# Kernel tuning notes

Measured on AMD Instinct MI355X. Metric: run time of the kernel, lower is better.

## Reference

```python
import jax, jax.numpy as jnp
import numpy as np

D_MODEL = 256
NS = 8


def _linear_params(key, out_f, in_f):
    s = 1.0 / np.sqrt(in_f)
    kw, kb = jax.random.split(key)
    W = jax.random.uniform(kw, (out_f, in_f), jnp.float32, -s, s)
    b = jax.random.uniform(kb, (out_f,), jnp.float32, -s, s)
    return W, b


def setup_inputs() -> dict:
    key = jax.random.key(0)
    ks = jax.random.split(key, 8)
    B, NQ = 2, 10000
    C, D, H, W = D_MODEL, 16, 64, 64
    Wdp, bdp = _linear_params(ks[3], NS * 3, D_MODEL)
    Wa, ba = _linear_params(ks[4], NS, D_MODEL)
    Wv, bv = _linear_params(ks[5], D_MODEL, D_MODEL)
    Ww, bw = _linear_params(ks[6], D_MODEL, D_MODEL)
    Wo, bo = _linear_params(ks[7], D_MODEL, D_MODEL)
    return {
        "query": jax.random.normal(ks[0], (B, NQ, D_MODEL), jnp.float32),
        "ref_points": jax.random.uniform(ks[1], (B, NQ, 3), jnp.float32, -1.0, 1.0),
        "image_features": jax.random.normal(ks[2], (B, C, D, H, W), jnp.float32),
        "mask": jnp.ones((B, 2, NQ), dtype=bool),
        "Wdp": Wdp, "bdp": bdp,
        "Wa": Wa, "ba": ba,
        "Wv": Wv, "bv": bv,
        "Ww": Ww, "bw": bw,
        "Wo": Wo, "bo": bo,
    }


def grid_sample_3d(vol, grid):
    """Trilinear grid_sample, align_corners=True, zero padding.
    vol: (B,C,D,H,W); grid: (B,N,P,3) with (x,y,z) in [-1,1] (x indexes W).
    Returns (B,N,P,C)."""
    B, C, D, H, W = vol.shape
    vol_t = jnp.transpose(vol, (0, 2, 3, 4, 1))  # (B,D,H,W,C)
    ix = (grid[..., 0] + 1.0) * 0.5 * (W - 1)
    iy = (grid[..., 1] + 1.0) * 0.5 * (H - 1)
    iz = (grid[..., 2] + 1.0) * 0.5 * (D - 1)
    x0 = jnp.floor(ix); y0 = jnp.floor(iy); z0 = jnp.floor(iz)
    fx = ix - x0; fy = iy - y0; fz = iz - z0

    def gather(v, zi, yi, xi):  # v: (D,H,W,C); indices (N,P)
        return v[zi, yi, xi]  # (N,P,C)

    out = jnp.zeros(grid.shape[:-1] + (C,), vol.dtype)
    for dz in (0, 1):
        for dy in (0, 1):
            for dx in (0, 1):
                xi = x0 + dx; yi = y0 + dy; zi = z0 + dz
                w = ((fx if dx else 1.0 - fx)
                     * (fy if dy else 1.0 - fy)
                     * (fz if dz else 1.0 - fz))
                valid = ((xi >= 0) & (xi <= W - 1)
                         & (yi >= 0) & (yi <= H - 1)
                         & (zi >= 0) & (zi <= D - 1))
                xc = jnp.clip(xi, 0, W - 1).astype(jnp.int32)
                yc = jnp.clip(yi, 0, H - 1).astype(jnp.int32)
                zc = jnp.clip(zi, 0, D - 1).astype(jnp.int32)
                vals = jax.vmap(gather)(vol_t, zc, yc, xc)  # (B,N,P,C)
                out = out + (w * valid)[..., None] * vals
    return out


def reference(query, ref_points, image_features, mask,
              Wdp, bdp, Wa, ba, Wv, bv, Ww, bw, Wo, bo):
    B, NQ, C = query.shape
    n_points = NS
    # learned offsets around reference points
    delta_p = (query @ Wdp.T + bdp).reshape(B, NQ, n_points, 3)
    p_delta_p = ref_points[:, :, None, :] + delta_p
    # reorder dims [1,0,2] -> grid (x,y,z) convention of grid_sample
    grid = p_delta_p[..., jnp.array([1, 0, 2])]
    sampled = grid_sample_3d(image_features, grid)  # (B,NQ,Ns,C)
    v = sampled @ Wv.T + bv          # value_proj
    wv = v @ Ww.T + bw               # W
    attn = jax.nn.softmax(query @ Wa.T + ba, axis=-1)  # (B,NQ,Ns)
    summed = jnp.einsum('bnpc,bnp->bnc', wv, attn)
    m = jnp.any(mask, axis=1)  # (B,NQ)
    summed = summed * m[..., None]
    return summed @ Wo.T + bo
```

## Files before the change

### kernel.cpp

```cpp
#include <hip/hip_runtime.h>

#define NQ    10000
#define BATCH 2
#define CDIM  256
#define DD    16
#define HH    64
#define WW    64

using bf16x8 = __attribute__((ext_vector_type(8))) short;
using f32x4  = __attribute__((ext_vector_type(4))) float;

__device__ __forceinline__ unsigned short f2bf(float f) {
    unsigned int u = __float_as_uint(f);
    u = u + 0x7FFFu + ((u >> 16) & 1u);
    return (unsigned short)(u >> 16);
}
__device__ __forceinline__ float bf2f(unsigned short h) {
    return __uint_as_float(((unsigned int)h) << 16);
}

__global__ __launch_bounds__(256) void k_transpose_bf16(const float* __restrict__ vol,
                                                        unsigned short* __restrict__ volt) {
    __shared__ float tile[64][65];
    int bid  = blockIdx.x;
    int cblk = bid & 3;
    int y    = (bid >> 2) & 63;
    int z    = (bid >> 8) & 15;
    int b    = bid >> 12;
    int tid  = threadIdx.x;
    int lx   = tid & 63, wy = tid >> 6;

    const float* src = vol + (size_t)(b * CDIM + cblk * 64) * (DD * HH * WW)
                           + (size_t)z * (HH * WW) + y * WW;
#pragma unroll
    for (int i = 0; i < 16; ++i) {
        int cl = wy * 16 + i;
        tile[cl][lx] = src[(size_t)cl * (DD * HH * WW) + lx];
    }
    __syncthreads();
    unsigned int* dst32 = reinterpret_cast<unsigned int*>(
        volt + ((size_t)(b * DD + z) * HH + y) * WW * CDIM) + cblk * 32;
    int cp = tid & 31;
#pragma unroll
    for (int i = 0; i < 8; ++i) {
        int x = i * 8 + (tid >> 5);
        unsigned int uo = (unsigned int)f2bf(tile[cp * 2][x])
                        | ((unsigned int)f2bf(tile[cp * 2 + 1][x]) << 16);
        dst32[(size_t)x * (CDIM / 2) + cp] = uo;
    }
}

template <bool BF16OUT>
__global__ __launch_bounds__(256) void k_combine(const float* __restrict__ A,
                                                 const float* __restrict__ B,
                                                 const float* __restrict__ bin,
                                                 const float* __restrict__ badd,
                                                 void* __restrict__ outW,
                                                 float* __restrict__ outb) {
    int i = blockIdx.x, j = threadIdx.x;
    __shared__ __align__(16) float row[256];
    __shared__ float red[4];
    row[j] = A[i * 256 + j];
    __syncthreads();
    float a0 = 0.f, a1 = 0.f, a2 = 0.f, a3 = 0.f;
#pragma unroll 4
    for (int k = 0; k < 256; k += 4) {
        a0 = fmaf(row[k + 0], B[(k + 0) * 256 + j], a0);
        a1 = fmaf(row[k + 1], B[(k + 1) * 256 + j], a1);
        a2 = fmaf(row[k + 2], B[(k + 2) * 256 + j], a2);
        a3 = fmaf(row[k + 3], B[(k + 3) * 256 + j], a3);
    }
    float acc = (a0 + a1) + (a2 + a3);
    if (BF16OUT)
        ((unsigned short*)outW)[i * 256 + j] = f2bf(acc);
    else
        ((float*)outW)[i * 256 + j] = acc;

    float pb = row[j] * bin[j];
    for (int off = 32; off; off >>= 1) pb += __shfl_down(pb, off, 64);
    int lane = j & 63, wv_ = j >> 6;
    if (lane == 0) red[wv_] = pb;
    __syncthreads();
    if (j == 0) outb[i] = red[0] + red[1] + red[2] + red[3] + badd[i];
}

__device__ __forceinline__ void geom_issue(
    int p, const float* __restrict__ dotsw, const float* __restrict__ bdp,
    float r0, float r1, float r2, float a,
    const ushort4* __restrict__ vb4, int lane,
    ushort4 (&u)[8], float (&wt)[8]) {
    float ix = fmaf(r1 + dotsw[p * 3 + 1] + bdp[p * 3 + 1], 31.5f, 31.5f);
    float iy = fmaf(r0 + dotsw[p * 3 + 0] + bdp[p * 3 + 0], 31.5f, 31.5f);
    float iz = fmaf(r2 + dotsw[p * 3 + 2] + bdp[p * 3 + 2], 7.5f, 7.5f);
    float xf = floorf(ix), yf = floorf(iy), zf = floorf(iz);
    float fx = ix - xf, fy = iy - yf, fz = iz - zf;
    int x0 = (int)xf, y0 = (int)yf, z0 = (int)zf;
    int xc[2], yc[2], zc[2];
    float wx[2], wy2[2], wz2[2];
#pragma unroll
    for (int d = 0; d < 2; ++d) {
        int xi = x0 + d, yi = y0 + d, zi = z0 + d;
        wx[d]  = (xi >= 0 && xi < WW) ? (d ? fx : 1.f - fx) : 0.f;
        wy2[d] = (yi >= 0 && yi < HH) ? (d ? fy : 1.f - fy) : 0.f;
        wz2[d] = ((zi >= 0 && zi < DD) ? (d ? fz : 1.f - fz) : 0.f) * a;
        xc[d] = min(max(xi, 0), WW - 1);
        yc[d] = min(max(yi, 0), HH - 1);
        zc[d] = min(max(zi, 0), DD - 1);
    }
    float wzy[4];
#pragma unroll
    for (int zz = 0; zz < 2; ++zz)
#pragma unroll
        for (int yy = 0; yy < 2; ++yy) wzy[zz * 2 + yy] = wz2[zz] * wy2[yy];
#pragma unroll
    for (int c = 0; c < 8; ++c) {
        int dz = c >> 2, dy = (c >> 1) & 1, dx = c & 1;
        wt[c] = wzy[dz * 2 + dy] * wx[dx];
        int off = (zc[dz] * HH + yc[dy]) * WW + xc[dx];
        off = __builtin_amdgcn_readfirstlane(off);
        u[c] = vb4[(size_t)off * (CDIM / 4) + lane];
    }
}

__device__ __forceinline__ void proc8(const ushort4 (&u)[8], const float (&wt)[8],
                                      float4& acc) {
#pragma unroll
    for (int c = 0; c < 8; ++c) {
        acc.x = fmaf(wt[c], bf2f(u[c].x), acc.x);
        acc.y = fmaf(wt[c], bf2f(u[c].y), acc.y);
        acc.z = fmaf(wt[c], bf2f(u[c].z), acc.z);
        acc.w = fmaf(wt[c], bf2f(u[c].w), acc.w);
    }
}

template <bool USE_VOLT>
__global__ __launch_bounds__(256) void k_sample4(
    const float* __restrict__ query, const float* __restrict__ refp,
    const float* __restrict__ vol, const unsigned short* __restrict__ voltb,
    const float* __restrict__ Wdp, const float* __restrict__ bdp,
    const float* __restrict__ Wa, const float* __restrict__ ba,
    unsigned short* __restrict__ S) {
    int tid = threadIdx.x, w = tid >> 6, lane = tid & 63;
    int g = lane >> 4, ch = lane & 15;
    int bq0 = blockIdx.x * 4;
    __shared__ float dots[4][32];

    {
        float4 qv[4][4];
#pragma unroll
        for (int q = 0; q < 4; ++q)
#pragma unroll
            for (int i = 0; i < 4; ++i)
                qv[q][i] = *reinterpret_cast<const float4*>(
                    query + (size_t)(bq0 + q) * 256 + ch * 16 + i * 4);
#pragma unroll
        for (int rr = 0; rr < 2; ++rr) {
            int row = w * 8 + rr * 4 + g;
            const float* rp = (row < 24) ? (Wdp + row * 256) : (Wa + (row - 24) * 256);
            float4 wv4[4];
#pragma unroll
            for (int i = 0; i < 4; ++i)
                wv4[i] = *reinterpret_cast<const float4*>(rp + ch * 16 + i * 4);
#pragma unroll
            for (int q = 0; q < 4; ++q) {
                float s = 0.f;
#pragma unroll
                for (int i = 0; i < 4; ++i)
                    s = fmaf(wv4[i].x, qv[q][i].x, fmaf(wv4[i].y, qv[q][i].y,
                        fmaf(wv4[i].z, qv[q][i].z, fmaf(wv4[i].w, qv[q][i].w, s))));
                s += __shfl_xor(s, 1); s += __shfl_xor(s, 2);
                s += __shfl_xor(s, 4); s += __shfl_xor(s, 8);
                if (ch == q) dots[q][row] = s;
            }
        }
    }
    __syncthreads();

    int bq = bq0 + w, b = bq / NQ;
    const float* dotsw = dots[w];
    float lg[8]; float mx = -1e30f;
#pragma unroll
    for (int p = 0; p < 8; ++p) { lg[p] = dotsw[24 + p] + ba[p]; mx = fmaxf(mx, lg[p]); }
    float se = 0.f;
#pragma unroll
    for (int p = 0; p < 8; ++p) { lg[p] = __expf(lg[p] - mx); se += lg[p]; }
    float inv = 1.f / se;
    float r0 = refp[bq * 3 + 0], r1 = refp[bq * 3 + 1], r2 = refp[bq * 3 + 2];

    float4 acc = make_float4(0.f, 0.f, 0.f, 0.f);
    if (USE_VOLT) {
        const ushort4* vb4 = reinterpret_cast<const ushort4*>(
            voltb + (size_t)b * (DD * HH * WW) * CDIM);
        ushort4 u0[8], u1[8];
        float w0a[8], w1a[8];
        geom_issue(0, dotsw, bdp, r0, r1, r2, lg[0] * inv, vb4, lane, u0, w0a);
#pragma unroll
        for (int p = 0; p < 7; ++p) {
            if ((p & 1) == 0) {
                geom_issue(p + 1, dotsw, bdp, r0, r1, r2, lg[p + 1] * inv, vb4, lane, u1, w1a);
                proc8(u0, w0a, acc);
            } else {
                geom_issue(p + 1, dotsw, bdp, r0, r1, r2, lg[p + 1] * inv, vb4, lane, u0, w0a);
                proc8(u1, w1a, acc);
            }
        }
        proc8(u1, w1a, acc);
    } else {
        const float* vf = vol + (size_t)b * CDIM * (DD * HH * WW);
#pragma unroll
        for (int p = 0; p < 8; ++p) {
            float a = lg[p] * inv;
            float ix = fmaf(r1 + dotsw[p * 3 + 1] + bdp[p * 3 + 1], 31.5f, 31.5f);
            float iy = fmaf(r0 + dotsw[p * 3 + 0] + bdp[p * 3 + 0], 31.5f, 31.5f);
            float iz = fmaf(r2 + dotsw[p * 3 + 2] + bdp[p * 3 + 2], 7.5f, 7.5f);
            float xf = floorf(ix), yf = floorf(iy), zf = floorf(iz);
            float fx = ix - xf, fy = iy - yf, fz = iz - zf;
            int x0 = (int)xf, y0 = (int)yf, z0 = (int)zf;
            int xc[2], yc[2], zc[2]; float wx[2], wy2[2], wz2[2];
#pragma unroll
            for (int d = 0; d < 2; ++d) {
                int xi = x0 + d, yi = y0 + d, zi = z0 + d;
                wx[d]  = (xi >= 0 && xi < WW) ? (d ? fx : 1.f - fx) : 0.f;
                wy2[d] = (yi >= 0 && yi < HH) ? (d ? fy : 1.f - fy) : 0.f;
                wz2[d] = ((zi >= 0 && zi < DD) ? (d ? fz : 1.f - fz) : 0.f) * a;
                xc[d] = min(max(xi, 0), WW - 1);
                yc[d] = min(max(yi, 0), HH - 1);
                zc[d] = min(max(zi, 0), DD - 1);
            }
#pragma unroll
            for (int c = 0; c < 8; ++c) {
                int dz = c >> 2, dy = (c >> 1) & 1, dx = c & 1;
                float wgt = wz2[dz] * wy2[dy] * wx[dx];
                int off = (zc[dz] * HH + yc[dy]) * WW + xc[dx];
#pragma unroll
                for (int cc = 0; cc < 4; ++cc) {
                    float v = vf[(size_t)(lane * 4 + cc) * (DD * HH * WW) + off];
                    (&acc.x)[cc] = fmaf(wgt, v, (&acc.x)[cc]);
                }
            }
        }
    }
    ushort4 o;
    o.x = f2bf(acc.x); o.y = f2bf(acc.y); o.z = f2bf(acc.z); o.w = f2bf(acc.w);
    reinterpret_cast<ushort4*>(S + (size_t)bq * 256)[lane] = o;
}

__global__ __launch_bounds__(256) void k_gemm_mx(
    const unsigned short* __restrict__ A,
    const unsigned short* __restrict__ Bw,
    const float* __restrict__ bias,
    const float* __restrict__ bo,
    const int* __restrict__ mask,
    float* __restrict__ C, int M) {
    const int LDT = 40;
    __shared__ unsigned short As[64 * LDT];
    __shared__ unsigned short Bs[64 * LDT];
    int tid = threadIdx.x, wv = tid >> 6, lane = tid & 63;
    int row0 = blockIdx.x * 64, col0 = blockIdx.y * 64;
    int wr = (wv & 1) * 32, wc = (wv >> 1) * 32;
    f32x4 acc[2][2] = {};

    int sr = tid >> 2, skc = tid & 3;
    for (int k0 = 0; k0 < 256; k0 += 32) {
        int gr = row0 + sr;
        uint4 av = make_uint4(0u, 0u, 0u, 0u);
        if (gr < M)
            av = *reinterpret_cast<const uint4*>(A + (size_t)gr * 256 + k0 + skc * 8);
        *reinterpret_cast<uint4*>(&As[sr * LDT + skc * 8]) = av;
        uint4 bv = *reinterpret_cast<const uint4*>(Bw + (size_t)(col0 + sr) * 256 + k0 + skc * 8);
        *reinterpret_cast<uint4*>(&Bs[sr * LDT + skc * 8]) = bv;
        __syncthreads();
        bf16x8 af[2], bf[2];
#pragma unroll
        for (int mi = 0; mi < 2; ++mi)
            af[mi] = *reinterpret_cast<const bf16x8*>(
                &As[(wr + mi * 16 + (lane & 15)) * LDT + (lane >> 4) * 8]);
#pragma unroll
        for (int ni = 0; ni < 2; ++ni)
            bf[ni] = *reinterpret_cast<const bf16x8*>(
                &Bs[(wc + ni * 16 + (lane & 15)) * LDT + (lane >> 4) * 8]);
#pragma unroll
        for (int mi = 0; mi < 2; ++mi)
#pragma unroll
            for (int ni = 0; ni < 2; ++ni)
                acc[mi][ni] = __builtin_amdgcn_mfma_f32_16x16x32_bf16(
                    af[mi], bf[ni], acc[mi][ni], 0, 0, 0);
        __syncthreads();
    }

    int lc = lane & 15, lr4 = (lane >> 4) * 4;
    float biasv[2], bov[2];
#pragma unroll
    for (int ni = 0; ni < 2; ++ni) {
        int col = col0 + wc + ni * 16 + lc;
        biasv[ni] = bias[col];
        bov[ni]   = bo[col];
    }
#pragma unroll
    for (int mi = 0; mi < 2; ++mi)
#pragma unroll
        for (int r = 0; r < 4; ++r) {
            int row = row0 + wr + mi * 16 + lr4 + r;
            if (row >= M) continue;
            int b = row / NQ, q = row - b * NQ;
            bool mv = (mask[(b * 2 + 0) * NQ + q] | mask[(b * 2 + 1) * NQ + q]) != 0;
#pragma unroll
            for (int ni = 0; ni < 2; ++ni) {
                int col = col0 + wc + ni * 16 + lc;
                C[(size_t)row * 256 + col] = mv ? (acc[mi][ni][r] + biasv[ni]) : bov[ni];
            }
        }
}

extern "C" void kernel_launch(void* const* d_in, const int* in_sizes, int n_in,
                              void* d_out, int out_size, void* d_ws, size_t ws_size,
                              hipStream_t stream) {
    const float* query = (const float*)d_in[0];
    const float* refp  = (const float*)d_in[1];
    const float* vol   = (const float*)d_in[2];
    const int*   mask  = (const int*)d_in[3];
    const float* Wdp   = (const float*)d_in[4];
    const float* bdp   = (const float*)d_in[5];
    const float* Wa    = (const float*)d_in[6];
    const float* ba    = (const float*)d_in[7];
    const float* Wv    = (const float*)d_in[8];
    const float* bv    = (const float*)d_in[9];
    const float* Ww    = (const float*)d_in[10];
    const float* bw    = (const float*)d_in[11];
    const float* Wo    = (const float*)d_in[12];
    const float* bo    = (const float*)d_in[13];
    float* out = (float*)d_out;

    char* ws = (char*)d_ws;
    const size_t M = (size_t)BATCH * NQ;
    size_t o_S    = 0;
    size_t o_W12  = o_S + M * 256 * 2;
    size_t o_b12  = o_W12 + 256 * 256 * 4;
    size_t o_W123 = o_b12 + 1024;
    size_t o_b123 = o_W123 + 256 * 256 * 2;
    size_t o_volt = (o_b123 + 1024 + 255) & ~(size_t)255;
    size_t need_volt = o_volt + (size_t)BATCH * DD * HH * WW * CDIM * 2;
    bool use_volt = ws_size >= need_volt;

    unsigned short* Sb   = (unsigned short*)(ws + o_S);
    float*          W12  = (float*)(ws + o_W12);
    float*          b12  = (float*)(ws + o_b12);
    unsigned short* W123 = (unsigned short*)(ws + o_W123);
    float*          b123 = (float*)(ws + o_b123);
    unsigned short* volt = (unsigned short*)(ws + o_volt);

    if (use_volt)
        k_transpose_bf16<<<BATCH * DD * HH * (CDIM / 64), 256, 0, stream>>>(vol, volt);
    k_combine<false><<<256, 256, 0, stream>>>(Ww, Wv, bv, bw, W12, b12);
    k_combine<true ><<<256, 256, 0, stream>>>(Wo, W12, b12, bo, W123, b123);

    if (use_volt)
        k_sample4<true><<<(int)(M / 4), 256, 0, stream>>>(query, refp, vol, volt,
                                                          Wdp, bdp, Wa, ba, Sb);
    else
        k_sample4<false><<<(int)(M / 4), 256, 0, stream>>>(query, refp, vol, volt,
                                                           Wdp, bdp, Wa, ba, Sb);

    dim3 g((unsigned)((M + 63) / 64), 4);
    k_gemm_mx<<<g, 256, 0, stream>>>(Sb, W123, b123, bo, mask, out, (int)M);
}
```

Baseline: 134.4 us.

## Sort queries by spatial bin and swizzle blocks to improve gather locality

```diff
diff --git a/kernel.cpp b/kernel.cpp
--- a/kernel.cpp
+++ b/kernel.cpp
@@ -84,6 +84,45 @@
     if (j == 0) outb[i] = red[0] + red[1] + red[2] + red[3] + badd[i];
 }
 
+__global__ __launch_bounds__(256) void k_keys(const float* __restrict__ refp,
+                                              int* __restrict__ keys,
+                                              int* __restrict__ hist) {
+    int q = blockIdx.x * 256 + threadIdx.x;
+    if (q >= BATCH * NQ) return;
+    float r0 = refp[q * 3 + 0];
+    float r2 = refp[q * 3 + 2];
+    int iz = min(max((int)((r2 + 1.f) * 7.5f), 0), 15);
+    int iy = min(max((int)((r0 + 1.f) * 31.5f), 0), 63);
+    int key = (q / NQ) * 128 + iz * 8 + (iy >> 3);
+    keys[q] = key;
+    atomicAdd(&hist[key], 1);
+}
+
+__global__ __launch_bounds__(256) void k_scan(const int* __restrict__ hist,
+                                              int* __restrict__ offs) {
+    __shared__ int tmp[256];
+    int t = threadIdx.x;
+    int v = hist[t];
+    tmp[t] = v;
+    __syncthreads();
+    for (int d = 1; d < 256; d <<= 1) {
+        int add = (t >= d) ? tmp[t - d] : 0;
+        __syncthreads();
+        if (t >= d) tmp[t] += add;
+        __syncthreads();
+    }
+    offs[t] = tmp[t] - v;
+}
+
+__global__ __launch_bounds__(256) void k_scatter(const int* __restrict__ keys,
+                                                 int* __restrict__ offs,
+                                                 int* __restrict__ perm) {
+    int q = blockIdx.x * 256 + threadIdx.x;
+    if (q >= BATCH * NQ) return;
+    int slot = atomicAdd(&offs[keys[q]], 1);
+    perm[slot] = q;
+}
+
 __device__ __forceinline__ void geom_issue(
     int p, const float* __restrict__ dotsw, const float* __restrict__ bdp,
     float r0, float r1, float r2, float a,
@@ -134,15 +173,21 @@
 }
 
 template <bool USE_VOLT>
-__global__ __launch_bounds__(256) void k_sample4(
+__global__ __launch_bounds__(256) void k_sample4s(
     const float* __restrict__ query, const float* __restrict__ refp,
     const float* __restrict__ vol, const unsigned short* __restrict__ voltb,
     const float* __restrict__ Wdp, const float* __restrict__ bdp,
     const float* __restrict__ Wa, const float* __restrict__ ba,
+    const int* __restrict__ perm,
     unsigned short* __restrict__ S) {
     int tid = threadIdx.x, w = tid >> 6, lane = tid & 63;
     int g = lane >> 4, ch = lane & 15;
-    int bq0 = blockIdx.x * 4;
+    const int NWG = (BATCH * NQ) / 4;
+    int sbid = ((int)blockIdx.x & 7) * (NWG / 8) + ((int)blockIdx.x >> 3);
+    int bq0 = sbid * 4;
+    int pq[4];
+#pragma unroll
+    for (int q = 0; q < 4; ++q) pq[q] = perm[bq0 + q];
     __shared__ float dots[4][32];
 
     {
@@ -152,7 +197,7 @@
 #pragma unroll
             for (int i = 0; i < 4; ++i)
                 qv[q][i] = *reinterpret_cast<const float4*>(
-                    query + (size_t)(bq0 + q) * 256 + ch * 16 + i * 4);
+                    query + (size_t)pq[q] * 256 + ch * 16 + i * 4);
 #pragma unroll
         for (int rr = 0; rr < 2; ++rr) {
             int row = w * 8 + rr * 4 + g;
@@ -176,7 +221,7 @@
     }
     __syncthreads();
 
-    int bq = bq0 + w, b = bq / NQ;
+    int bq = pq[w], b = bq / NQ;
     const float* dotsw = dots[w];
     float lg[8]; float mx = -1e30f;
 #pragma unroll
@@ -338,7 +383,11 @@
     size_t o_b12  = o_W12 + 256 * 256 * 4;
     size_t o_W123 = o_b12 + 1024;
     size_t o_b123 = o_W123 + 256 * 256 * 2;
-    size_t o_volt = (o_b123 + 1024 + 255) & ~(size_t)255;
+    size_t o_keys = o_b123 + 1024;
+    size_t o_hist = o_keys + M * 4;
+    size_t o_offs = o_hist + 1024;
+    size_t o_perm = o_offs + 1024;
+    size_t o_volt = (o_perm + M * 4 + 255) & ~(size_t)255;
     size_t need_volt = o_volt + (size_t)BATCH * DD * HH * WW * CDIM * 2;
     bool use_volt = ws_size >= need_volt;
 
@@ -347,7 +396,17 @@
     float*          b12  = (float*)(ws + o_b12);
     unsigned short* W123 = (unsigned short*)(ws + o_W123);
     float*          b123 = (float*)(ws + o_b123);
+    int*            keys = (int*)(ws + o_keys);
+    int*            hist = (int*)(ws + o_hist);
+    int*            offs = (int*)(ws + o_offs);
+    int*            perm = (int*)(ws + o_perm);
     unsigned short* volt = (unsigned short*)(ws + o_volt);
+
+    hipMemsetAsync(hist, 0, 1024, stream);
+    int nqb = (int)((M + 255) / 256);
+    k_keys<<<nqb, 256, 0, stream>>>(refp, keys, hist);
+    k_scan<<<1, 256, 0, stream>>>(hist, offs);
+    k_scatter<<<nqb, 256, 0, stream>>>(keys, offs, perm);
 
     if (use_volt)
         k_transpose_bf16<<<BATCH * DD * HH * (CDIM / 64), 256, 0, stream>>>(vol, volt);
@@ -355,11 +414,11 @@
     k_combine<true ><<<256, 256, 0, stream>>>(Wo, W12, b12, bo, W123, b123);
 
     if (use_volt)
-        k_sample4<true><<<(int)(M / 4), 256, 0, stream>>>(query, refp, vol, volt,
-                                                          Wdp, bdp, Wa, ba, Sb);
+        k_sample4s<true><<<(int)(M / 4), 256, 0, stream>>>(query, refp, vol, volt,
+                                                           Wdp, bdp, Wa, ba, perm, Sb);
     else
-        k_sample4<false><<<(int)(M / 4), 256, 0, stream>>>(query, refp, vol, volt,
-                                                           Wdp, bdp, Wa, ba, Sb);
+        k_sample4s<false><<<(int)(M / 4), 256, 0, stream>>>(query, refp, vol, volt,
+                                                            Wdp, bdp, Wa, ba, perm, Sb);
 
     dim3 g((unsigned)((M + 63) / 64), 4);
     k_gemm_mx<<<g, 256, 0, stream>>>(Sb, W123, b123, bo, mask, out, (int)M);
```

New measurement: 159.3 us. 1.19x slower.
